# Performance work log

Hardware: AMD Instinct MI355X
Metric: run time of the kernel (lower is better)

Reference implementation:

```python
import jax, jax.numpy as jnp
import numpy as np

N, T, CUT = 64, 2, 25.0            # atoms, atom types, cutoff radius
ED = [3, 32, 64, 128]              # embedding MLP dims (input 3)
LD = [384, 256, 256, 128, 3]       # per-atom MLP dims (input 3*E)
P = T * (T + 1) // 2               # number of unordered type pairs
M = 27 * N                         # periodic images


def setup_inputs() -> dict:
    key = jax.random.key(0)
    ks = jax.random.split(key, 16)
    x = jax.random.uniform(ks[0], (N, 3), jnp.float32) * 10.0
    lattice = 10.0 * jnp.eye(3, dtype=jnp.float32)
    atom_types = (jnp.arange(N) % T).astype(jnp.int32)

    def lin(k, shape, fan_in):
        return jax.random.normal(k, shape, jnp.float32) / np.sqrt(fan_in)

    inp = {"x": x, "lattice": lattice}
    for i in range(3):
        inp[f"We{i+1}"] = lin(ks[1 + i], (P, ED[i], ED[i + 1]), ED[i])
        inp[f"be{i+1}"] = jnp.zeros((P, ED[i + 1]), jnp.float32)
    for i in range(4):
        inp[f"Wl{i+1}"] = lin(ks[5 + i], (N, LD[i], LD[i + 1]), LD[i])
        inp[f"bl{i+1}"] = jnp.zeros((N, LD[i + 1]), jnp.float32)
    inp["atom_types"] = atom_types
    return inp


def reference(x, lattice, We1, be1, We2, be2, We3, be3,
              Wl1, bl1, Wl2, bl2, Wl3, bl3, Wl4, bl4, atom_types):
    act = jax.nn.leaky_relu  # slope 0.01, matches nn.LeakyReLU default
    idx = jnp.arange(-1, 2, dtype=x.dtype)
    # (i,j,k) combos in the same loop order as torch (i slowest, k fastest)
    combos = jnp.stack(jnp.meshgrid(idx, idx, idx, indexing="ij"), -1).reshape(27, 3)
    x_ext = (x[None, :, :] + (combos @ lattice)[:, None, :]).reshape(M, 3)  # [M,3]
    # the in-place subtraction in torch telescopes: at step n, x_ext = x_ext0 - x_ext0[n]
    rel = x_ext[None, :, :] - x_ext[:N, None, :]                    # [N,M,3]
    dist = jnp.linalg.norm(rel, axis=-1)                            # [N,M]
    mask = dist <= CUT
    rank = jnp.cumsum(mask, axis=1) - 1
    # torch removes POSITION n of the compacted neighbor list -> rank == n
    keep = (mask & (rank != jnp.arange(N)[:, None])).astype(x.dtype)  # [N,M]

    types_ext = jnp.tile(atom_types, 27)                            # [M]
    lo = jnp.minimum(atom_types[:, None], types_ext[None, :])
    hi = jnp.maximum(atom_types[:, None], types_ext[None, :])
    pid = lo * T - (lo * (lo - 1)) // 2 + (hi - lo)                 # [N,M] pair-type id

    # run all P pair-type embedding MLPs on every candidate edge, then route
    h = act(jnp.einsum("nmi,pio->pnmo", rel, We1) + be1[:, None, None, :])
    h = act(jnp.einsum("pnmi,pio->pnmo", h, We2) + be2[:, None, None, :])
    h = act(jnp.einsum("pnmi,pio->pnmo", h, We3) + be3[:, None, None, :])
    g = h[pid, jnp.arange(N)[:, None], jnp.arange(M)[None, :], :]   # [N,M,E]

    # d_n = g_n^T @ x_n over kept neighbors; row-major flatten of [E,3] -> [3E]
    d = jnp.einsum("nm,nme,nmc->nec", keep, g, rel).reshape(N, -1)  # [N,3E]

    h = act(jnp.einsum("ni,nio->no", d, Wl1) + bl1)
    h = act(jnp.einsum("ni,nio->no", h, Wl2) + bl2)
    h = act(jnp.einsum("ni,nio->no", h, Wl3) + bl3)
    out = jnp.einsum("ni,nio->no", h, Wl4) + bl4                    # [N,3]
    out = out - jnp.mean(out, axis=0, keepdims=True)
    return out.reshape(-1)                                          # [3N]
```

## Files before the change

### kernel.cpp

```cpp
#include <hip/hip_runtime.h>

#define LEAKY(t) ((t) > 0.0f ? (t) : 0.01f*(t))

typedef __attribute__((ext_vector_type(8))) short short8;
typedef __attribute__((ext_vector_type(4))) float floatx4;

static __device__ __forceinline__ short f2bf(float f) {
  unsigned u = __float_as_uint(f);
  u += 0x7FFFu + ((u >> 16) & 1u);
  return (short)(u >> 16);
}


__global__ __launch_bounds__(256) void prep_kernel(
    const float* __restrict__ We1, const float* __restrict__ be1,
    const float* __restrict__ We2, const float* __restrict__ We3,
    short* __restrict__ g_WT)
{
  const int gt = blockIdx.x * 256 + threadIdx.x;
  const int GS = gridDim.x * 256;
  for (int it = gt; it < 4224; it += GS) {
    short8 v;
    if (it < 384) {
      const int p = it >> 7, r = it & 127, ot = (r >> 6) & 1, ln = r & 63;
      const int col = ln & 15, quad = ln >> 4, o = ot * 16 + col;
      #pragma unroll
      for (int j = 0; j < 8; ++j) {
        const int k = quad * 8 + j;
        float f = 0.0f;
        if (k < 3) f = We1[p * 96 + k * 32 + o];
        else if (k == 3) f = be1[p * 32 + o];
        v[j] = f2bf(f);
      }
    } else if (it < 1152) {
      const int t = it - 384;
      const int p = t >> 8, r = t & 255, ot = r >> 6, ln = r & 63;
      const int col = ln & 15, quad = ln >> 4, o = ot * 16 + col;
      #pragma unroll
      for (int j = 0; j < 8; ++j) {
        const int k = quad * 8 + j;
        v[j] = f2bf(We2[p * 2048 + k * 64 + o]);
      }
    } else {
      const int t = it - 1152;
      const int p = t >> 10, r = t & 1023, ot = r >> 7, rr = r & 127;
      const int ks = rr >> 6, ln = rr & 63;
      const int col = ln & 15, quad = ln >> 4, o = ot * 16 + col;
      #pragma unroll
      for (int j = 0; j < 8; ++j) {
        const int k = ks * 32 + quad * 8 + j;
        v[j] = f2bf(We3[p * 8192 + k * 128 + o]);
      }
    }
    *(short8*)(g_WT + it * 8) = v;
  }
}

__global__ __launch_bounds__(256, 4) void embed_kernel(
    const float* __restrict__ x, const float* __restrict__ lattice,
    const short* __restrict__ g_WT,
    const float* __restrict__ be2, const float* __restrict__ be3,
    const int* __restrict__ types, float* __restrict__ dpart)
{
  __shared__ __align__(16) float rel4[144 * 4];
  __shared__ __align__(16) float rk4[144 * 4];
  __shared__ __align__(16) short h1s[144 * 40];
  __shared__ __align__(16) short h2s[144 * 72];

  const int n = blockIdx.x, par = blockIdx.y, chunk = blockIdx.z;
  const int tid = threadIdx.x;
  const int lane = tid & 63, w = tid >> 6;
  const int col = lane & 15, quad = lane >> 4;

  const int tn = types[n];
  const int tj = types[par];
  const int lo = tn < tj ? tn : tj;
  const int hi = tn < tj ? tj : tn;
  const int p  = lo * 2 - (lo * (lo - 1)) / 2 + (hi - lo);

  const short8* WT8 = (const short8*)g_WT;
  const short8 w1b0 = WT8[(p * 2 + 0) * 64 + lane];
  const short8 w1b1 = WT8[(p * 2 + 1) * 64 + lane];
  short8 w2b[4];
  #pragma unroll
  for (int ot = 0; ot < 4; ++ot) w2b[ot] = WT8[384 + (p * 4 + ot) * 64 + lane];
  short8 w3b[2][2];
  #pragma unroll
  for (int nt = 0; nt < 2; ++nt)
    #pragma unroll
    for (int ks = 0; ks < 2; ++ks)
      w3b[nt][ks] = WT8[1152 + ((p * 8 + 2 * w + nt) * 2 + ks) * 64 + lane];
  float bias2[4];
  #pragma unroll
  for (int ot = 0; ot < 4; ++ot) bias2[ot] = be2[p * 64 + ot * 16 + col];
  float bias3[2];
  #pragma unroll
  for (int nt = 0; nt < 2; ++nt) bias3[nt] = be3[p * 128 + w * 32 + nt * 16 + col];

  if (tid < 144) {
    const int q  = chunk * 144 + tid;
    const int c  = q >> 5;
    const int jj = q & 31;
    const int j  = 2 * jj + par;
    const float f0 = (float)(c / 9);
    const float f1 = (float)((c / 3) % 3);
    const float f2c = (float)(c % 3);
    const float rel0 = x[j*3+0] - x[n*3+0] + f0*lattice[0] + f1*lattice[3] + f2c*lattice[6];
    const float rel1 = x[j*3+1] - x[n*3+1] + f0*lattice[1] + f1*lattice[4] + f2c*lattice[7];
    const float rel2 = x[j*3+2] - x[n*3+2] + f0*lattice[2] + f1*lattice[5] + f2c*lattice[8];
    const float dist2 = rel0*rel0 + rel1*rel1 + rel2*rel2;
    const int m = c * 64 + j;
    const bool keep = (dist2 <= 625.0f) && (m != n);
    const float kf = keep ? 1.0f : 0.0f;
    rel4[tid*4+0] = rel0; rel4[tid*4+1] = rel1;
    rel4[tid*4+2] = rel2; rel4[tid*4+3] = 1.0f;
    rk4[tid*4+0] = rel0*kf; rk4[tid*4+1] = rel1*kf;
    rk4[tid*4+2] = rel2*kf; rk4[tid*4+3] = 0.0f;
  }
  __syncthreads();

  for (int mt = w; mt < 9; mt += 4) {
    const float4 r4 = *(const float4*)&rel4[(mt*16 + col) * 4];
    short8 a = {0, 0, 0, 0, 0, 0, 0, 0};
    if (quad == 0) {
      a[0] = f2bf(r4.x); a[1] = f2bf(r4.y); a[2] = f2bf(r4.z);
      a[3] = (short)0x3F80;
    }
    const floatx4 z = {0.f, 0.f, 0.f, 0.f};
    const floatx4 c0 = __builtin_amdgcn_mfma_f32_16x16x32_bf16(a, w1b0, z, 0, 0, 0);
    const floatx4 c1 = __builtin_amdgcn_mfma_f32_16x16x32_bf16(a, w1b1, z, 0, 0, 0);
    #pragma unroll
    for (int r = 0; r < 4; ++r) {
      const int pair = mt*16 + quad*4 + r;
      h1s[pair*40 +      col] = f2bf(LEAKY(c0[r]));
      h1s[pair*40 + 16 + col] = f2bf(LEAKY(c1[r]));
    }
    const short8 a2 = *(const short8*)&h1s[(mt*16 + col) * 40 + quad*8];
    #pragma unroll
    for (int ot = 0; ot < 4; ++ot) {
      floatx4 acc = {bias2[ot], bias2[ot], bias2[ot], bias2[ot]};
      acc = __builtin_amdgcn_mfma_f32_16x16x32_bf16(a2, w2b[ot], acc, 0, 0, 0);
      #pragma unroll
      for (int r = 0; r < 4; ++r) {
        const int pair = mt*16 + quad*4 + r;
        h2s[pair*72 + ot*16 + col] = f2bf(LEAKY(acc[r]));
      }
    }
  }
  __syncthreads();

  float vacc[2][3] = {{0,0,0},{0,0,0}};
  for (int mt = 0; mt < 9; ++mt) {
    const short8 a0 = *(const short8*)&h2s[(mt*16 + col) * 72 +      quad*8];
    const short8 a1 = *(const short8*)&h2s[(mt*16 + col) * 72 + 32 + quad*8];
    float4 rks[4];
    #pragma unroll
    for (int r = 0; r < 4; ++r)
      rks[r] = *(const float4*)&rk4[(mt*16 + quad*4 + r) * 4];
    #pragma unroll
    for (int nt = 0; nt < 2; ++nt) {
      floatx4 acc = {bias3[nt], bias3[nt], bias3[nt], bias3[nt]};
      acc = __builtin_amdgcn_mfma_f32_16x16x32_bf16(a0, w3b[nt][0], acc, 0, 0, 0);
      acc = __builtin_amdgcn_mfma_f32_16x16x32_bf16(a1, w3b[nt][1], acc, 0, 0, 0);
      #pragma unroll
      for (int r = 0; r < 4; ++r) {
        const float h3 = LEAKY(acc[r]);
        vacc[nt][0] += h3 * rks[r].x;
        vacc[nt][1] += h3 * rks[r].y;
        vacc[nt][2] += h3 * rks[r].z;
      }
    }
  }
  #pragma unroll
  for (int nt = 0; nt < 2; ++nt)
    #pragma unroll
    for (int c = 0; c < 3; ++c) {
      float v = vacc[nt][c];
      v += __shfl_xor(v, 16, 64);
      v += __shfl_xor(v, 32, 64);
      vacc[nt][c] = v;
    }
  if (lane < 32) {
    const int nts = lane >> 4, colw = lane & 15;
    const int o = w*32 + nts*16 + colw;
    const int slot = par * 6 + chunk;
    float* dst = dpart + ((size_t)(slot * 64 + n)) * 384 + o * 3;
    #pragma unroll
    for (int c = 0; c < 3; ++c)
      dst[c] = nts ? vacc[1][c] : vacc[0][c];
  }
}

__global__ __launch_bounds__(1024) void fit_kernel(
    const float* __restrict__ dpart,
    const float* __restrict__ W1, const float* __restrict__ b1,
    const float* __restrict__ W2, const float* __restrict__ b2,
    const float* __restrict__ W3, const float* __restrict__ b3,
    const float* __restrict__ W4, const float* __restrict__ b4,
    float* __restrict__ pre)
{
  __shared__ __align__(16) float a0[384];
  __shared__ __align__(16) float a1[256];
  __shared__ __align__(16) float a2[256];
  __shared__ __align__(16) float a3[128];
  __shared__ __align__(16) floatx4 red[1024];
  const int n = blockIdx.x, tid = threadIdx.x;

  if (tid < 384) {
    float s = 0.f;
    #pragma unroll
    for (int sl = 0; sl < 12; ++sl)
      s += dpart[((size_t)(sl * 64 + n)) * 384 + tid];
    a0[tid] = s;
  }
  __syncthreads();

  {
    const int g = tid & 63, s = tid >> 6;
    const float* Wp = W1 + (size_t)n * 98304 + 4 * g;
    floatx4 acc = {0.f, 0.f, 0.f, 0.f};
    #pragma unroll 8
    for (int k = 0; k < 24; ++k) {
      const int i = s * 24 + k;
      acc += a0[i] * *(const floatx4*)(Wp + (size_t)i * 256);
    }
    red[tid] = acc;
    __syncthreads();
    if (tid < 64) {
      floatx4 v = red[tid];
      #pragma unroll
      for (int s2 = 1; s2 < 16; ++s2) v += red[s2 * 64 + tid];
      const float4 bb = *(const float4*)&b1[n * 256 + 4 * tid];
      a1[4*tid+0] = LEAKY(v[0] + bb.x);
      a1[4*tid+1] = LEAKY(v[1] + bb.y);
      a1[4*tid+2] = LEAKY(v[2] + bb.z);
      a1[4*tid+3] = LEAKY(v[3] + bb.w);
    }
    __syncthreads();
  }

  {
    const int g = tid & 63, s = tid >> 6;
    const float* Wp = W2 + (size_t)n * 65536 + 4 * g;
    floatx4 acc = {0.f, 0.f, 0.f, 0.f};
    #pragma unroll 8
    for (int k = 0; k < 16; ++k) {
      const int i = s * 16 + k;
      acc += a1[i] * *(const floatx4*)(Wp + (size_t)i * 256);
    }
    red[tid] = acc;
    __syncthreads();
    if (tid < 64) {
      floatx4 v = red[tid];
      #pragma unroll
      for (int s2 = 1; s2 < 16; ++s2) v += red[s2 * 64 + tid];
      const float4 bb = *(const float4*)&b2[n * 256 + 4 * tid];
      a2[4*tid+0] = LEAKY(v[0] + bb.x);
      a2[4*tid+1] = LEAKY(v[1] + bb.y);
      a2[4*tid+2] = LEAKY(v[2] + bb.z);
      a2[4*tid+3] = LEAKY(v[3] + bb.w);
    }
    __syncthreads();
  }

  {
    const int g = tid & 31, s = tid >> 5;
    const float* Wp = W3 + (size_t)n * 32768 + 4 * g;
    floatx4 acc = {0.f, 0.f, 0.f, 0.f};
    #pragma unroll
    for (int k = 0; k < 8; ++k) {
      const int i = s * 8 + k;
      acc += a2[i] * *(const floatx4*)(Wp + (size_t)i * 128);
    }
    red[tid] = acc;
    __syncthreads();
    if (tid < 32) {
      floatx4 v = red[tid];
      #pragma unroll
      for (int s2 = 1; s2 < 32; ++s2) v += red[s2 * 32 + tid];
      const float4 bb = *(const float4*)&b3[n * 128 + 4 * tid];
      a3[4*tid+0] = LEAKY(v[0] + bb.x);
      a3[4*tid+1] = LEAKY(v[1] + bb.y);
      a3[4*tid+2] = LEAKY(v[2] + bb.z);
      a3[4*tid+3] = LEAKY(v[3] + bb.w);
    }
    __syncthreads();
  }

  {
    float* redf = (float*)red;
    if (tid < 128) {
      const float hv = a3[tid];
      const float* W4n = W4 + (size_t)n * 384;
      float p0 = hv * W4n[tid*3 + 0];
      float p1 = hv * W4n[tid*3 + 1];
      float p2 = hv * W4n[tid*3 + 2];
      #pragma unroll
      for (int off = 32; off >= 1; off >>= 1) {
        p0 += __shfl_down(p0, off, 64);
        p1 += __shfl_down(p1, off, 64);
        p2 += __shfl_down(p2, off, 64);
      }
      if ((tid & 63) == 0) {
        const int wv = tid >> 6;
        redf[wv*3 + 0] = p0; redf[wv*3 + 1] = p1; redf[wv*3 + 2] = p2;
      }
    }
    __syncthreads();
    if (tid < 3)
      pre[n*3 + tid] = redf[tid] + redf[3 + tid] + b4[n*3 + tid];
  }
}

__global__ __launch_bounds__(256) void mean_kernel(
    const float* __restrict__ pre, float* __restrict__ out)
{
  __shared__ float sp[192];
  __shared__ float meanv[3];
  const int tid = threadIdx.x;
  if (tid < 192) sp[tid] = pre[tid];
  __syncthreads();
  if (tid < 3) {
    float s = 0.f;
    #pragma unroll
    for (int nn = 0; nn < 64; ++nn) s += sp[nn*3 + tid];
    meanv[tid] = s * (1.0f / 64.0f);
  }
  __syncthreads();
  if (tid < 192) out[tid] = sp[tid] - meanv[tid % 3];
}

extern "C" void kernel_launch(void* const* d_in, const int* in_sizes, int n_in,
                              void* d_out, int out_size, void* d_ws, size_t ws_size,
                              hipStream_t stream) {
  const float* x       = (const float*)d_in[0];
  const float* lattice = (const float*)d_in[1];
  const float* We1 = (const float*)d_in[2];
  const float* be1 = (const float*)d_in[3];
  const float* We2 = (const float*)d_in[4];
  const float* be2 = (const float*)d_in[5];
  const float* We3 = (const float*)d_in[6];
  const float* be3 = (const float*)d_in[7];
  const float* Wl1 = (const float*)d_in[8];
  const float* bl1 = (const float*)d_in[9];
  const float* Wl2 = (const float*)d_in[10];
  const float* bl2 = (const float*)d_in[11];
  const float* Wl3 = (const float*)d_in[12];
  const float* bl3 = (const float*)d_in[13];
  const float* Wl4 = (const float*)d_in[14];
  const float* bl4 = (const float*)d_in[15];
  const int*   types = (const int*)d_in[16];

  float* wsf   = (float*)d_ws;
  float* dpart = wsf;
  float* pre   = wsf + 294912;
  short* g_WT  = (short*)(wsf + 295104);

  prep_kernel<<<17, 256, 0, stream>>>(We1, be1, We2, We3, g_WT);
  embed_kernel<<<dim3(64, 2, 6), 256, 0, stream>>>(
      x, lattice, g_WT, be2, be3, types, dpart);
  fit_kernel<<<64, 1024, 0, stream>>>(
      dpart, Wl1, bl1, Wl2, bl2, Wl3, bl3, Wl4, bl4, pre);
  mean_kernel<<<1, 256, 0, stream>>>(pre, (float*)d_out);
}
```

Measured before the change: 137.3 us.

## Split per-atom fitting MLP into three kernels with output-quarter grid parallelism

Replaces the single fit kernel (64 blocks of 1024 threads, one per atom) with three launches. The first two layers each run on a 64x4 grid where every block computes a quarter of the outputs, and the last two layers run in a 512-thread kernel. Intermediate activations pass through global workspace. The aim is to spread the weight-streaming GEMVs across more blocks and compute units to raise memory bandwidth use, at the cost of two extra launches, global round-trips and a tree reduction with more barriers.

After: 134.9 us. No clear change (-1.8%).

```diff
diff --git a/kernel.cpp b/kernel.cpp
--- a/kernel.cpp
+++ b/kernel.cpp
@@ -191,93 +191,114 @@
   }
 }
 
-__global__ __launch_bounds__(1024) void fit_kernel(
+__global__ __launch_bounds__(256) void fitA_kernel(
     const float* __restrict__ dpart,
     const float* __restrict__ W1, const float* __restrict__ b1,
+    float* __restrict__ h1out)
+{
+  __shared__ float a0[384];
+  __shared__ floatx4 red[256];
+  const int n = blockIdx.x, oq = blockIdx.y, tid = threadIdx.x;
+  for (int i = tid; i < 384; i += 256) {
+    float s = 0.f;
+    #pragma unroll
+    for (int sl = 0; sl < 12; ++sl)
+      s += dpart[((size_t)(sl * 64 + n)) * 384 + i];
+    a0[i] = s;
+  }
+  __syncthreads();
+  const int g = tid & 15, s = tid >> 4;
+  const float* Wp = W1 + (size_t)n * 98304 + oq * 64 + 4 * g;
+  floatx4 acc = {0.f, 0.f, 0.f, 0.f};
+  #pragma unroll 12
+  for (int k = 0; k < 24; ++k) {
+    const int i = s * 24 + k;
+    acc += a0[i] * *(const floatx4*)(Wp + (size_t)i * 256);
+  }
+  red[tid] = acc;
+  __syncthreads();
+  #pragma unroll
+  for (int off = 128; off >= 16; off >>= 1) {
+    if (tid < off) red[tid] += red[tid + off];
+    __syncthreads();
+  }
+  if (tid < 16) {
+    const floatx4 v = red[tid];
+    const int o = oq * 64 + 4 * tid;
+    const float4 bb = *(const float4*)&b1[n * 256 + o];
+    float4 r;
+    r.x = LEAKY(v[0] + bb.x); r.y = LEAKY(v[1] + bb.y);
+    r.z = LEAKY(v[2] + bb.z); r.w = LEAKY(v[3] + bb.w);
+    *(float4*)&h1out[n * 256 + o] = r;
+  }
+}
+
+__global__ __launch_bounds__(256) void fitB_kernel(
+    const float* __restrict__ in,
     const float* __restrict__ W2, const float* __restrict__ b2,
+    float* __restrict__ out)
+{
+  __shared__ float din[256];
+  __shared__ floatx4 red[256];
+  const int n = blockIdx.x, oq = blockIdx.y, tid = threadIdx.x;
+  din[tid] = in[n * 256 + tid];
+  __syncthreads();
+  const int g = tid & 15, s = tid >> 4;
+  const float* Wp = W2 + (size_t)n * 65536 + oq * 64 + 4 * g;
+  floatx4 acc = {0.f, 0.f, 0.f, 0.f};
+  #pragma unroll
+  for (int k = 0; k < 16; ++k) {
+    const int i = s * 16 + k;
+    acc += din[i] * *(const floatx4*)(Wp + (size_t)i * 256);
+  }
+  red[tid] = acc;
+  __syncthreads();
+  #pragma unroll
+  for (int off = 128; off >= 16; off >>= 1) {
+    if (tid < off) red[tid] += red[tid + off];
+    __syncthreads();
+  }
+  if (tid < 16) {
+    const floatx4 v = red[tid];
+    const int o = oq * 64 + 4 * tid;
+    const float4 bb = *(const float4*)&b2[n * 256 + o];
+    float4 r;
+    r.x = LEAKY(v[0] + bb.x); r.y = LEAKY(v[1] + bb.y);
+    r.z = LEAKY(v[2] + bb.z); r.w = LEAKY(v[3] + bb.w);
+    *(float4*)&out[n * 256 + o] = r;
+  }
+}
+
+__global__ __launch_bounds__(512) void fitC_kernel(
+    const float* __restrict__ in,
     const float* __restrict__ W3, const float* __restrict__ b3,
     const float* __restrict__ W4, const float* __restrict__ b4,
     float* __restrict__ pre)
 {
-  __shared__ __align__(16) float a0[384];
-  __shared__ __align__(16) float a1[256];
-  __shared__ __align__(16) float a2[256];
-  __shared__ __align__(16) float a3[128];
-  __shared__ __align__(16) floatx4 red[1024];
+  __shared__ float din[256];
+  __shared__ float a3[128];
+  __shared__ __align__(16) floatx4 red[512];
   const int n = blockIdx.x, tid = threadIdx.x;
-
-  if (tid < 384) {
-    float s = 0.f;
-    #pragma unroll
-    for (int sl = 0; sl < 12; ++sl)
-      s += dpart[((size_t)(sl * 64 + n)) * 384 + tid];
-    a0[tid] = s;
-  }
-  __syncthreads();
-
+  if (tid < 256) din[tid] = in[n * 256 + tid];
+  __syncthreads();
   {
-    const int g = tid & 63, s = tid >> 6;
-    const float* Wp = W1 + (size_t)n * 98304 + 4 * g;
-    floatx4 acc = {0.f, 0.f, 0.f, 0.f};
-    #pragma unroll 8
-    for (int k = 0; k < 24; ++k) {
-      const int i = s * 24 + k;
-      acc += a0[i] * *(const floatx4*)(Wp + (size_t)i * 256);
-    }
-    red[tid] = acc;
-    __syncthreads();
-    if (tid < 64) {
-      floatx4 v = red[tid];
-      #pragma unroll
-      for (int s2 = 1; s2 < 16; ++s2) v += red[s2 * 64 + tid];
-      const float4 bb = *(const float4*)&b1[n * 256 + 4 * tid];
-      a1[4*tid+0] = LEAKY(v[0] + bb.x);
-      a1[4*tid+1] = LEAKY(v[1] + bb.y);
-      a1[4*tid+2] = LEAKY(v[2] + bb.z);
-      a1[4*tid+3] = LEAKY(v[3] + bb.w);
-    }
-    __syncthreads();
-  }
-
-  {
-    const int g = tid & 63, s = tid >> 6;
-    const float* Wp = W2 + (size_t)n * 65536 + 4 * g;
+    const int g = tid & 31, s = tid >> 5;
+    const float* Wp = W3 + (size_t)n * 32768 + 4 * g;
     floatx4 acc = {0.f, 0.f, 0.f, 0.f};
     #pragma unroll 8
     for (int k = 0; k < 16; ++k) {
       const int i = s * 16 + k;
-      acc += a1[i] * *(const floatx4*)(Wp + (size_t)i * 256);
+      acc += din[i] * *(const floatx4*)(Wp + (size_t)i * 128);
     }
     red[tid] = acc;
     __syncthreads();
-    if (tid < 64) {
-      floatx4 v = red[tid];
-      #pragma unroll
-      for (int s2 = 1; s2 < 16; ++s2) v += red[s2 * 64 + tid];
-      const float4 bb = *(const float4*)&b2[n * 256 + 4 * tid];
-      a2[4*tid+0] = LEAKY(v[0] + bb.x);
-      a2[4*tid+1] = LEAKY(v[1] + bb.y);
-      a2[4*tid+2] = LEAKY(v[2] + bb.z);
-      a2[4*tid+3] = LEAKY(v[3] + bb.w);
-    }
-    __syncthreads();
-  }
-
-  {
-    const int g = tid & 31, s = tid >> 5;
-    const float* Wp = W3 + (size_t)n * 32768 + 4 * g;
-    floatx4 acc = {0.f, 0.f, 0.f, 0.f};
-    #pragma unroll
-    for (int k = 0; k < 8; ++k) {
-      const int i = s * 8 + k;
-      acc += a2[i] * *(const floatx4*)(Wp + (size_t)i * 128);
-    }
-    red[tid] = acc;
-    __syncthreads();
+    #pragma unroll
+    for (int off = 256; off >= 32; off >>= 1) {
+      if (tid < off) red[tid] += red[tid + off];
+      __syncthreads();
+    }
     if (tid < 32) {
-      floatx4 v = red[tid];
-      #pragma unroll
-      for (int s2 = 1; s2 < 32; ++s2) v += red[s2 * 32 + tid];
+      const floatx4 v = red[tid];
       const float4 bb = *(const float4*)&b3[n * 128 + 4 * tid];
       a3[4*tid+0] = LEAKY(v[0] + bb.x);
       a3[4*tid+1] = LEAKY(v[1] + bb.y);
@@ -286,7 +307,6 @@
     }
     __syncthreads();
   }
-
   {
     float* redf = (float*)red;
     if (tid < 128) {
@@ -353,13 +373,16 @@
 
   float* wsf   = (float*)d_ws;
   float* dpart = wsf;
-  float* pre   = wsf + 294912;
-  short* g_WT  = (short*)(wsf + 295104);
+  float* h1f   = wsf + 294912;
+  float* h2f   = wsf + 311296;
+  float* pre   = wsf + 327680;
+  short* g_WT  = (short*)(wsf + 327872);
 
   prep_kernel<<<17, 256, 0, stream>>>(We1, be1, We2, We3, g_WT);
   embed_kernel<<<dim3(64, 2, 6), 256, 0, stream>>>(
       x, lattice, g_WT, be2, be3, types, dpart);
-  fit_kernel<<<64, 1024, 0, stream>>>(
-      dpart, Wl1, bl1, Wl2, bl2, Wl3, bl3, Wl4, bl4, pre);
+  fitA_kernel<<<dim3(64, 4), 256, 0, stream>>>(dpart, Wl1, bl1, h1f);
+  fitB_kernel<<<dim3(64, 4), 256, 0, stream>>>(h1f, Wl2, bl2, h2f);
+  fitC_kernel<<<64, 512, 0, stream>>>(h2f, Wl3, bl3, Wl4, bl4, pre);
   mean_kernel<<<1, 256, 0, stream>>>(pre, (float*)d_out);
 }
```
